# Optimization experiments

Measured on AMD Instinct MI355X. Metric: run time of the kernel, lower is better.

## Reference

```python
import jax, jax.numpy as jnp
import numpy as np

S, N, H = 4096, 32, 512

def setup_inputs() -> dict:
    key = jax.random.key(0)
    ks = jax.random.split(key, 8)
    scale = 1.0 / np.sqrt(H)
    return {
        "hidden": jax.random.normal(ks[0], (N, H), dtype=jnp.float32),
        "encoder_outputs": jax.random.normal(ks[1], (S, N, H), dtype=jnp.float32),
        "W_w": jax.random.uniform(ks[2], (H, H), jnp.float32, -scale, scale),
        "W_b": jax.random.uniform(ks[3], (H,), jnp.float32, -scale, scale),
        "U_w": jax.random.uniform(ks[4], (H, H), jnp.float32, -scale, scale),
        "U_b": jax.random.uniform(ks[5], (H,), jnp.float32, -scale, scale),
        "v_w": jax.random.uniform(ks[6], (1, H), jnp.float32, -scale, scale),
        "v_b": jax.random.uniform(ks[7], (1,), jnp.float32, -scale, scale),
    }

def reference(hidden, encoder_outputs, W_w, W_b, U_w, U_b, v_w, v_b):
    # W(hidden): [N,H] -> broadcast over seq dim (equivalent to expand then Linear)
    wh = hidden @ W_w.T + W_b                      # [N, H]
    ue = jnp.einsum('snh,kh->snk', encoder_outputs, U_w) + U_b  # [S, N, H]
    energy = jnp.tanh(wh[None, :, :] + ue)         # [S, N, H]
    score = jnp.einsum('snh,oh->sno', energy, v_w) + v_b        # [S, N, 1]
    attention_weights = jax.nn.softmax(score, axis=0)           # softmax over seq
    context = jnp.sum(attention_weights * encoder_outputs, axis=0)  # [N, H]
    return (context, attention_weights)
```

## Files before the change

kernel.cpp:

```cpp
#include <hip/hip_runtime.h>
#include <hip/hip_bf16.h>

#define Sdim 4096
#define Ndim 32
#define Hdim 512
#define Mdim (Sdim * Ndim)

#define BM 128
#define BN 256
#define BK 32

typedef __bf16 bf16x8 __attribute__((ext_vector_type(8)));
typedef float f32x4 __attribute__((ext_vector_type(4)));
typedef unsigned short ushort8v __attribute__((ext_vector_type(8)));

__device__ __forceinline__ void load_lds16(const void* g, void* l) {
    __builtin_amdgcn_global_load_lds(
        (const __attribute__((address_space(1))) void*)g,
        (__attribute__((address_space(3))) void*)l, 16, 0, 0);
}

__device__ __forceinline__ float ftanh(float x) {
    float e = __expf(2.f * x);
    return 1.f - 2.f / (e + 1.f);
}

__global__ __launch_bounds__(256) void k_prep_bias(
    const float* __restrict__ hidden, const float* __restrict__ Ww,
    const float* __restrict__ Wb, const float* __restrict__ Ubias,
    float* __restrict__ bias) {
    const int t = threadIdx.x, w = t >> 6, lane = t & 63;
    const int cc = blockIdx.x * 4 + w;
    const float4 w0 = *(const float4*)(Ww + (size_t)cc * Hdim + lane * 8);
    const float4 w1 = *(const float4*)(Ww + (size_t)cc * Hdim + lane * 8 + 4);
    const float wb = Wb[cc] + Ubias[cc];
    for (int n = 0; n < Ndim; ++n) {
        const float4 h0 = *(const float4*)(hidden + n * Hdim + lane * 8);
        const float4 h1 = *(const float4*)(hidden + n * Hdim + lane * 8 + 4);
        float p = w0.x * h0.x + w0.y * h0.y + w0.z * h0.z + w0.w * h0.w +
                  w1.x * h1.x + w1.y * h1.y + w1.z * h1.z + w1.w * h1.w;
        p += __shfl_xor(p, 1);  p += __shfl_xor(p, 2);
        p += __shfl_xor(p, 4);  p += __shfl_xor(p, 8);
        p += __shfl_xor(p, 16); p += __shfl_xor(p, 32);
        if (lane == 0) bias[n * Hdim + cc] = p + wb;
    }
}

__global__ __launch_bounds__(256) void k_cvt(
    const float* __restrict__ src, unsigned short* __restrict__ dst) {
    const int i = blockIdx.x * 256 + threadIdx.x;
    float4 v = ((const float4*)src)[i];
    union { __hip_bfloat162 h[2]; ushort4 u; } r;
    r.h[0] = __float22bfloat162_rn(make_float2(v.x, v.y));
    r.h[1] = __float22bfloat162_rn(make_float2(v.z, v.w));
    ((ushort4*)dst)[i] = r.u;
}

__global__ __launch_bounds__(512, 4) void k_gemm_score(
    const float* __restrict__ enc,
    const unsigned short* __restrict__ Ub,
    const float* __restrict__ bias,
    const float* __restrict__ vw,
    float* __restrict__ scorep) {
    __shared__ __align__(16) unsigned short Asm[BM][40];
    __shared__ __align__(16) unsigned short Bsm[BN * BK];
    __shared__ float ssm[4][BM];

    const int t = threadIdx.x;
    const int lane = t & 63;
    const int w = t >> 6;
    const int wM = w >> 2;
    const int wN = w & 3;
    const int c = lane & 15;
    const int q = lane >> 4;

    const int rowblk = blockIdx.x >> 1;
    const int colblk = blockIdx.x & 1;
    const int mBase = rowblk * BM;
    const int colBase = colblk * BN;

    const int ar = t >> 2;
    const int aq = t & 3;
    const int asw = ((ar >> 3) & 1) << 1;
    const float* aptr = enc + (size_t)(mBase + ar) * Hdim + aq * 8;
    unsigned short* awr = &Asm[ar][(aq ^ asw) * 8];

    const int bsw = (lane & 3) ^ ((lane >> 4) & 3);
    const unsigned short* bptr0 =
        Ub + (size_t)(colBase + w * 16 + (lane >> 2)) * Hdim + bsw * 8;
    const unsigned short* bptr1 =
        Ub + (size_t)(colBase + 128 + w * 16 + (lane >> 2)) * Hdim + bsw * 8;
    unsigned short* bdst0 = &Bsm[(w * 16) * BK];
    unsigned short* bdst1 = &Bsm[(128 + w * 16) * BK];

    const int sA = ((c >> 3) & 1) << 1;
    const int sB = c >> 2;

    f32x4 acc[4][4];
#pragma unroll
    for (int i = 0; i < 4; ++i)
#pragma unroll
        for (int j = 0; j < 4; ++j) acc[i][j] = (f32x4){0.f, 0.f, 0.f, 0.f};

    for (int kk = 0; kk < Hdim / BK; ++kk) {
        __syncthreads();
        const float4 f0 = *(const float4*)(aptr + kk * BK);
        const float4 f1 = *(const float4*)(aptr + kk * BK + 4);
        union { __hip_bfloat162 h[4]; ushort8v v; } pk;
        pk.h[0] = __float22bfloat162_rn(make_float2(f0.x, f0.y));
        pk.h[1] = __float22bfloat162_rn(make_float2(f0.z, f0.w));
        pk.h[2] = __float22bfloat162_rn(make_float2(f1.x, f1.y));
        pk.h[3] = __float22bfloat162_rn(make_float2(f1.z, f1.w));
        *(ushort8v*)awr = pk.v;
        load_lds16(bptr0 + kk * BK, bdst0);
        load_lds16(bptr1 + kk * BK, bdst1);
        __syncthreads();

        bf16x8 af[4], bfr[4];
#pragma unroll
        for (int mi = 0; mi < 4; ++mi)
            af[mi] = *(const bf16x8*)&Asm[wM * 64 + mi * 16 + c][(q ^ sA) * 8];
#pragma unroll
        for (int ni = 0; ni < 4; ++ni) {
            const int col = wN * 64 + ni * 16 + c;
            bfr[ni] = *(const bf16x8*)&Bsm[col * BK + (q ^ sB) * 8];
        }
#pragma unroll
        for (int mi = 0; mi < 4; ++mi)
#pragma unroll
            for (int ni = 0; ni < 4; ++ni)
                acc[mi][ni] = __builtin_amdgcn_mfma_f32_16x16x32_bf16(
                    af[mi], bfr[ni], acc[mi][ni], 0, 0, 0);
    }

    float vcol[4];
#pragma unroll
    for (int ni = 0; ni < 4; ++ni) vcol[ni] = vw[colBase + wN * 64 + ni * 16 + c];

#pragma unroll
    for (int mi = 0; mi < 4; ++mi) {
#pragma unroll
        for (int reg = 0; reg < 4; ++reg) {
            const int rl = wM * 64 + mi * 16 + q * 4 + reg;
            const int n = rl & 31;
            float p = 0.f;
#pragma unroll
            for (int ni = 0; ni < 4; ++ni) {
                const int col = colBase + wN * 64 + ni * 16 + c;
                float e = acc[mi][ni][reg] + bias[n * Hdim + col];
                p += vcol[ni] * ftanh(e);
            }
            p += __shfl_xor(p, 1);
            p += __shfl_xor(p, 2);
            p += __shfl_xor(p, 4);
            p += __shfl_xor(p, 8);
            if (c == 0) ssm[wN][rl] = p;
        }
    }
    __syncthreads();
    if (t < BM) {
        const int m = mBase + t;
        const float s = ssm[0][t] + ssm[1][t] + ssm[2][t] + ssm[3][t];
        scorep[colblk * Mdim + (m & 31) * Sdim + (m >> 5)] = s;
    }
}

__global__ __launch_bounds__(256) void k_softmax(
    const float* __restrict__ scorep,
    float* __restrict__ out_w) {
    const int n = blockIdx.x;
    const int t = threadIdx.x;
    const int w = t >> 6;
    __shared__ float row[Sdim];
    __shared__ float red[8];
    const float4* s0 = (const float4*)(scorep + n * Sdim);
    const float4* s1 = (const float4*)(scorep + Mdim + n * Sdim);

    float mx = -1e30f;
    for (int i = t; i < Sdim / 4; i += 256) {
        float4 a = s0[i], b = s1[i];
        float4 v;
        v.x = a.x + b.x; v.y = a.y + b.y; v.z = a.z + b.z; v.w = a.w + b.w;
        ((float4*)row)[i] = v;
        mx = fmaxf(mx, fmaxf(fmaxf(v.x, v.y), fmaxf(v.z, v.w)));
    }
#pragma unroll
    for (int o = 32; o > 0; o >>= 1) mx = fmaxf(mx, __shfl_xor(mx, o));
    if ((t & 63) == 0) red[w] = mx;
    __syncthreads();
    mx = fmaxf(fmaxf(red[0], red[1]), fmaxf(red[2], red[3]));

    float sum = 0.f;
    for (int i = t; i < Sdim; i += 256) sum += __expf(row[i] - mx);
#pragma unroll
    for (int o = 32; o > 0; o >>= 1) sum += __shfl_xor(sum, o);
    if ((t & 63) == 0) red[4 + w] = sum;
    __syncthreads();
    sum = red[4] + red[5] + red[6] + red[7];
    const float inv = 1.f / sum;
    for (int i = t; i < Sdim; i += 256)
        out_w[i * Ndim + n] = __expf(row[i] - mx) * inv;
}

__global__ __launch_bounds__(256) void k_context(
    const float* __restrict__ enc, const float* __restrict__ wts,
    float* __restrict__ part) {
    const int n = blockIdx.x & 31;
    const int sc = blockIdx.x >> 5;
    const int s0 = sc * 256;
    const int t = threadIdx.x;
    const int hv = t & 127;
    const int sl = t >> 7;
    float4 a0 = {0.f, 0.f, 0.f, 0.f}, a1 = {0.f, 0.f, 0.f, 0.f};
    for (int i = sl * 2; i < 256; i += 4) {
        const float w0 = wts[(size_t)(s0 + i) * Ndim + n];
        const float w1 = wts[(size_t)(s0 + i + 1) * Ndim + n];
        const float4 e0 =
            *(const float4*)(enc + ((size_t)(s0 + i) * Ndim + n) * Hdim + hv * 4);
        const float4 e1 =
            *(const float4*)(enc + ((size_t)(s0 + i + 1) * Ndim + n) * Hdim + hv * 4);
        a0.x += w0 * e0.x; a0.y += w0 * e0.y; a0.z += w0 * e0.z; a0.w += w0 * e0.w;
        a1.x += w1 * e1.x; a1.y += w1 * e1.y; a1.z += w1 * e1.z; a1.w += w1 * e1.w;
    }
    a0.x += a1.x; a0.y += a1.y; a0.z += a1.z; a0.w += a1.w;
    __shared__ float4 red[128];
    if (sl == 1) red[hv] = a0;
    __syncthreads();
    if (sl == 0) {
        const float4 b = red[hv];
        float4 r;
        r.x = a0.x + b.x; r.y = a0.y + b.y; r.z = a0.z + b.z; r.w = a0.w + b.w;
        *(float4*)(part + (size_t)(sc * 32 + n) * Hdim + hv * 4) = r;
    }
}

__global__ __launch_bounds__(256) void k_ctx_reduce(
    const float* __restrict__ part, float* __restrict__ out) {
    const int j = blockIdx.x * 256 + threadIdx.x;
    float4 s = {0.f, 0.f, 0.f, 0.f};
    for (int i = 0; i < 16; ++i) {
        const float4 v = ((const float4*)part)[i * 4096 + j];
        s.x += v.x; s.y += v.y; s.z += v.z; s.w += v.w;
    }
    ((float4*)out)[j] = s;
}

extern "C" void kernel_launch(void* const* d_in, const int* in_sizes, int n_in,
                              void* d_out, int out_size, void* d_ws,
                              size_t ws_size, hipStream_t stream) {
    const float* hidden = (const float*)d_in[0];
    const float* enc    = (const float*)d_in[1];
    const float* Ww     = (const float*)d_in[2];
    const float* Wb     = (const float*)d_in[3];
    const float* Uw     = (const float*)d_in[4];
    const float* Ubias  = (const float*)d_in[5];
    const float* vw     = (const float*)d_in[6];

    float* out = (float*)d_out;

    char* ws = (char*)d_ws;
    float* bias          = (float*)(ws);
    unsigned short* Ub16 = (unsigned short*)(ws + (64 << 10));
    float* scorep        = (float*)(ws + (576 << 10));
    float* part          = (float*)(ws + (64 << 10));

    k_prep_bias<<<128, 256, 0, stream>>>(hidden, Ww, Wb, Ubias, bias);
    k_cvt<<<256, 256, 0, stream>>>(Uw, Ub16);
    k_gemm_score<<<(Mdim / BM) * 2, 512, 0, stream>>>(enc, Ub16, bias, vw,
                                                      scorep);
    k_softmax<<<Ndim, 256, 0, stream>>>(scorep, out + Ndim * Hdim);
    k_context<<<Ndim * (Sdim / 256), 256, 0, stream>>>(enc, out + Ndim * Hdim,
                                                       part);
    k_ctx_reduce<<<16, 256, 0, stream>>>(part, out);
}
```

Baseline: 537.1 us.

## Drop LDS staging in score GEMM and load MFMA fragments directly from global

The score GEMM no longer stages tiles in shared memory. Each wave loads its A fragments from fp32 global memory, converts them to bf16 in registers, and loads B fragments directly, with no per-K-step barriers. Block tile shrinks to 64 rows by 256 columns, using 256 threads and twice as many blocks. This removes synchronisation and LDS traffic, but the 4 waves now share no data, so each reloads the same A rows (4x redundant fp32 reads) and uncoalesced 16-byte strided loads rely on cache. The context kernel also unrolls its sequence loop by 4 to expose more memory-level parallelism.

After: 729.1 us. 1.36x slower.

```diff
diff --git a/kernel.cpp b/kernel.cpp
--- a/kernel.cpp
+++ b/kernel.cpp
@@ -6,19 +6,8 @@
 #define Hdim 512
 #define Mdim (Sdim * Ndim)
 
-#define BM 128
-#define BN 256
-#define BK 32
-
 typedef __bf16 bf16x8 __attribute__((ext_vector_type(8)));
 typedef float f32x4 __attribute__((ext_vector_type(4)));
-typedef unsigned short ushort8v __attribute__((ext_vector_type(8)));
-
-__device__ __forceinline__ void load_lds16(const void* g, void* l) {
-    __builtin_amdgcn_global_load_lds(
-        (const __attribute__((address_space(1))) void*)g,
-        (__attribute__((address_space(3))) void*)l, 16, 0, 0);
-}
 
 __device__ __forceinline__ float ftanh(float x) {
     float e = __expf(2.f * x);
@@ -56,45 +45,33 @@
     ((ushort4*)dst)[i] = r.u;
 }
 
-__global__ __launch_bounds__(512, 4) void k_gemm_score(
+__global__ __launch_bounds__(256, 3) void k_gemm_score(
     const float* __restrict__ enc,
     const unsigned short* __restrict__ Ub,
     const float* __restrict__ bias,
     const float* __restrict__ vw,
     float* __restrict__ scorep) {
-    __shared__ __align__(16) unsigned short Asm[BM][40];
-    __shared__ __align__(16) unsigned short Bsm[BN * BK];
-    __shared__ float ssm[4][BM];
+    __shared__ float ssm[4][64];
 
     const int t = threadIdx.x;
     const int lane = t & 63;
     const int w = t >> 6;
-    const int wM = w >> 2;
-    const int wN = w & 3;
     const int c = lane & 15;
     const int q = lane >> 4;
 
     const int rowblk = blockIdx.x >> 1;
     const int colblk = blockIdx.x & 1;
-    const int mBase = rowblk * BM;
-    const int colBase = colblk * BN;
-
-    const int ar = t >> 2;
-    const int aq = t & 3;
-    const int asw = ((ar >> 3) & 1) << 1;
-    const float* aptr = enc + (size_t)(mBase + ar) * Hdim + aq * 8;
-    unsigned short* awr = &Asm[ar][(aq ^ asw) * 8];
-
-    const int bsw = (lane & 3) ^ ((lane >> 4) & 3);
-    const unsigned short* bptr0 =
-        Ub + (size_t)(colBase + w * 16 + (lane >> 2)) * Hdim + bsw * 8;
-    const unsigned short* bptr1 =
-        Ub + (size_t)(colBase + 128 + w * 16 + (lane >> 2)) * Hdim + bsw * 8;
-    unsigned short* bdst0 = &Bsm[(w * 16) * BK];
-    unsigned short* bdst1 = &Bsm[(128 + w * 16) * BK];
-
-    const int sA = ((c >> 3) & 1) << 1;
-    const int sB = c >> 2;
+    const int mBase = rowblk * 64;
+    const int colBase = colblk * 256 + w * 64;
+
+    const float* aP[4];
+    const unsigned short* bP[4];
+#pragma unroll
+    for (int mi = 0; mi < 4; ++mi)
+        aP[mi] = enc + (size_t)(mBase + mi * 16 + c) * Hdim + q * 8;
+#pragma unroll
+    for (int ni = 0; ni < 4; ++ni)
+        bP[ni] = Ub + (size_t)(colBase + ni * 16 + c) * Hdim + q * 8;
 
     f32x4 acc[4][4];
 #pragma unroll
@@ -102,29 +79,23 @@
 #pragma unroll
         for (int j = 0; j < 4; ++j) acc[i][j] = (f32x4){0.f, 0.f, 0.f, 0.f};
 
-    for (int kk = 0; kk < Hdim / BK; ++kk) {
-        __syncthreads();
-        const float4 f0 = *(const float4*)(aptr + kk * BK);
-        const float4 f1 = *(const float4*)(aptr + kk * BK + 4);
-        union { __hip_bfloat162 h[4]; ushort8v v; } pk;
-        pk.h[0] = __float22bfloat162_rn(make_float2(f0.x, f0.y));
-        pk.h[1] = __float22bfloat162_rn(make_float2(f0.z, f0.w));
-        pk.h[2] = __float22bfloat162_rn(make_float2(f1.x, f1.y));
-        pk.h[3] = __float22bfloat162_rn(make_float2(f1.z, f1.w));
-        *(ushort8v*)awr = pk.v;
-        load_lds16(bptr0 + kk * BK, bdst0);
-        load_lds16(bptr1 + kk * BK, bdst1);
-        __syncthreads();
-
+#pragma unroll 2
+    for (int kk = 0; kk < Hdim / 32; ++kk) {
         bf16x8 af[4], bfr[4];
 #pragma unroll
-        for (int mi = 0; mi < 4; ++mi)
-            af[mi] = *(const bf16x8*)&Asm[wM * 64 + mi * 16 + c][(q ^ sA) * 8];
-#pragma unroll
-        for (int ni = 0; ni < 4; ++ni) {
-            const int col = wN * 64 + ni * 16 + c;
-            bfr[ni] = *(const bf16x8*)&Bsm[col * BK + (q ^ sB) * 8];
+        for (int mi = 0; mi < 4; ++mi) {
+            const float4 f0 = *(const float4*)(aP[mi] + kk * 32);
+            const float4 f1 = *(const float4*)(aP[mi] + kk * 32 + 4);
+            union { __hip_bfloat162 h[4]; bf16x8 v; } pk;
+            pk.h[0] = __float22bfloat162_rn(make_float2(f0.x, f0.y));
+            pk.h[1] = __float22bfloat162_rn(make_float2(f0.z, f0.w));
+            pk.h[2] = __float22bfloat162_rn(make_float2(f1.x, f1.y));
+            pk.h[3] = __float22bfloat162_rn(make_float2(f1.z, f1.w));
+            af[mi] = pk.v;
         }
+#pragma unroll
+        for (int ni = 0; ni < 4; ++ni)
+            bfr[ni] = *(const bf16x8*)(bP[ni] + kk * 32);
 #pragma unroll
         for (int mi = 0; mi < 4; ++mi)
 #pragma unroll
@@ -135,18 +106,18 @@
 
     float vcol[4];
 #pragma unroll
-    for (int ni = 0; ni < 4; ++ni) vcol[ni] = vw[colBase + wN * 64 + ni * 16 + c];
+    for (int ni = 0; ni < 4; ++ni) vcol[ni] = vw[colBase + ni * 16 + c];
 
 #pragma unroll
     for (int mi = 0; mi < 4; ++mi) {
 #pragma unroll
         for (int reg = 0; reg < 4; ++reg) {
-            const int rl = wM * 64 + mi * 16 + q * 4 + reg;
+            const int rl = mi * 16 + q * 4 + reg;
             const int n = rl & 31;
             float p = 0.f;
 #pragma unroll
             for (int ni = 0; ni < 4; ++ni) {
-                const int col = colBase + wN * 64 + ni * 16 + c;
+                const int col = colBase + ni * 16 + c;
                 float e = acc[mi][ni][reg] + bias[n * Hdim + col];
                 p += vcol[ni] * ftanh(e);
             }
@@ -154,11 +125,11 @@
             p += __shfl_xor(p, 2);
             p += __shfl_xor(p, 4);
             p += __shfl_xor(p, 8);
-            if (c == 0) ssm[wN][rl] = p;
+            if (c == 0) ssm[w][rl] = p;
         }
     }
     __syncthreads();
-    if (t < BM) {
+    if (t < 64) {
         const int m = mBase + t;
         const float s = ssm[0][t] + ssm[1][t] + ssm[2][t] + ssm[3][t];
         scorep[colblk * Mdim + (m & 31) * Sdim + (m >> 5)] = s;
@@ -212,17 +183,23 @@
     const int hv = t & 127;
     const int sl = t >> 7;
     float4 a0 = {0.f, 0.f, 0.f, 0.f}, a1 = {0.f, 0.f, 0.f, 0.f};
-    for (int i = sl * 2; i < 256; i += 4) {
+    float4 a2 = {0.f, 0.f, 0.f, 0.f}, a3 = {0.f, 0.f, 0.f, 0.f};
+    for (int i = sl * 4; i < 256; i += 8) {
         const float w0 = wts[(size_t)(s0 + i) * Ndim + n];
         const float w1 = wts[(size_t)(s0 + i + 1) * Ndim + n];
-        const float4 e0 =
-            *(const float4*)(enc + ((size_t)(s0 + i) * Ndim + n) * Hdim + hv * 4);
-        const float4 e1 =
-            *(const float4*)(enc + ((size_t)(s0 + i + 1) * Ndim + n) * Hdim + hv * 4);
+        const float w2 = wts[(size_t)(s0 + i + 2) * Ndim + n];
+        const float w3 = wts[(size_t)(s0 + i + 3) * Ndim + n];
+        const float4 e0 = *(const float4*)(enc + ((size_t)(s0 + i) * Ndim + n) * Hdim + hv * 4);
+        const float4 e1 = *(const float4*)(enc + ((size_t)(s0 + i + 1) * Ndim + n) * Hdim + hv * 4);
+        const float4 e2 = *(const float4*)(enc + ((size_t)(s0 + i + 2) * Ndim + n) * Hdim + hv * 4);
+        const float4 e3 = *(const float4*)(enc + ((size_t)(s0 + i + 3) * Ndim + n) * Hdim + hv * 4);
         a0.x += w0 * e0.x; a0.y += w0 * e0.y; a0.z += w0 * e0.z; a0.w += w0 * e0.w;
         a1.x += w1 * e1.x; a1.y += w1 * e1.y; a1.z += w1 * e1.z; a1.w += w1 * e1.w;
-    }
-    a0.x += a1.x; a0.y += a1.y; a0.z += a1.z; a0.w += a1.w;
+        a2.x += w2 * e2.x; a2.y += w2 * e2.y; a2.z += w2 * e2.z; a2.w += w2 * e2.w;
+        a3.x += w3 * e3.x; a3.y += w3 * e3.y; a3.z += w3 * e3.z; a3.w += w3 * e3.w;
+    }
+    a0.x += a1.x + a2.x + a3.x; a0.y += a1.y + a2.y + a3.y;
+    a0.z += a1.z + a2.z + a3.z; a0.w += a1.w + a2.w + a3.w;
     __shared__ float4 red[128];
     if (sl == 1) red[hv] = a0;
     __syncthreads();
@@ -266,7 +243,7 @@
 
     k_prep_bias<<<128, 256, 0, stream>>>(hidden, Ww, Wb, Ubias, bias);
     k_cvt<<<256, 256, 0, stream>>>(Uw, Ub16);
-    k_gemm_score<<<(Mdim / BM) * 2, 512, 0, stream>>>(enc, Ub16, bias, vw,
+    k_gemm_score<<<(Mdim / 64) * 2, 256, 0, stream>>>(enc, Ub16, bias, vw,
                                                       scorep);
     k_softmax<<<Ndim, 256, 0, stream>>>(scorep, out + Ndim * Hdim);
     k_context<<<Ndim * (Sdim / 256), 256, 0, stream>>>(enc, out + Ndim * Hdim,
```
